# Optimization experiments

Measured on AMD Instinct MI355X. Metric: run time of the kernel, lower is better.

The kernel has to match this reference:

```python
import jax, jax.numpy as jnp
import numpy as np

NEG_SLOPE = 0.2
TAU_MRF = 1.0
N_NODES = 100000
PROJ_DIM = 128
GAT_DIM = 64
N_EDGES = 1000000


def setup_inputs() -> dict:
    key = jax.random.key(0)
    ks = jax.random.split(key, 8)
    z_beh = jax.random.normal(ks[0], (N_NODES, PROJ_DIM), dtype=jnp.float32)
    z_pref = jax.random.normal(ks[1], (N_NODES, PROJ_DIM), dtype=jnp.float32)
    edge_index = jax.random.randint(ks[2], (2, N_EDGES), 0, N_NODES, dtype=jnp.int64)
    # xavier_uniform for [GAT_DIM, PROJ_DIM] linear weights
    lim_w = float(np.sqrt(6.0 / (PROJ_DIM + GAT_DIM)))
    W_b = jax.random.uniform(ks[3], (GAT_DIM, PROJ_DIM), minval=-lim_w, maxval=lim_w, dtype=jnp.float32)
    W_p = jax.random.uniform(ks[4], (GAT_DIM, PROJ_DIM), minval=-lim_w, maxval=lim_w, dtype=jnp.float32)
    # xavier_uniform on view(1, 2D): fan_in=1? torch treats [1, 2D] -> fan_in=2D, fan_out=1
    lim_a = float(np.sqrt(6.0 / (1 + 2 * GAT_DIM)))
    a_b = jax.random.uniform(ks[5], (2 * GAT_DIM,), minval=-lim_a, maxval=lim_a, dtype=jnp.float32)
    a_p = jax.random.uniform(ks[6], (2 * GAT_DIM,), minval=-lim_a, maxval=lim_a, dtype=jnp.float32)
    gamma_b = jnp.zeros((), dtype=jnp.float32)
    gamma_p = jnp.zeros((), dtype=jnp.float32)
    return {"z_beh": z_beh, "z_pref": z_pref, "W_b": W_b, "W_p": W_p,
            "a_b": a_b, "a_p": a_p, "gamma_b": gamma_b, "gamma_p": gamma_p,
            "edge_index_undirected": edge_index}


def _sym_score(h, a, src, dst, neg_slope):
    # e_ij = leaky_relu((cat[h_src, h_dst]) . a). Split a to avoid materializing
    # the [E, 2D] concat: dot each node once, then gather scalars per edge.
    D = h.shape[-1]
    si = h @ a[:D]   # [N] contribution of left slot
    sj = h @ a[D:]   # [N] contribution of right slot
    e_ij = jax.nn.leaky_relu(si[src] + sj[dst], negative_slope=neg_slope)
    e_ji = jax.nn.leaky_relu(si[dst] + sj[src], negative_slope=neg_slope)
    return 0.5 * (e_ij + e_ji)


def reference(z_beh, z_pref, W_b, W_p, a_b, a_p, gamma_b, gamma_p, edge_index_undirected):
    src = edge_index_undirected[0]
    dst = edge_index_undirected[1]
    h_b = z_beh @ W_b.T   # [N, D]
    h_p = z_pref @ W_p.T  # [N, D]
    s_b = _sym_score(h_b, a_b, src, dst, NEG_SLOPE)  # [E]
    s_p = _sym_score(h_p, a_p, src, dst, NEG_SLOPE)  # [E]
    w = jax.nn.softmax(jnp.stack([gamma_b, gamma_p]))
    s = w[0] * s_b + w[1] * s_p
    alpha_ij = jax.nn.sigmoid(s / TAU_MRF)
    return alpha_ij
```

## Files before the change

### kernel.cpp

```cpp
#include <hip/hip_runtime.h>
#include <hip/hip_bf16.h>

#define NEG_SLOPE 0.2f

typedef float f32x4 __attribute__((ext_vector_type(4)));

__device__ __forceinline__ unsigned f2bf(float f) {
    unsigned u = __float_as_uint(f);
    return (u + 0x7FFFu + ((u >> 16) & 1u)) >> 16;
}
__device__ __forceinline__ float bf2f(unsigned h) {
    return __uint_as_float(h << 16);
}

__device__ __forceinline__ float fold_reduce(float sib, float sjb,
                                             float sip, float sjp,
                                             bool hiB, bool hiJ) {
    float g1 = hiB ? sib : sip;
    float r1 = __shfl_xor(g1, 16);
    float acc_i = (hiB ? sip : sib) + r1;
    float g2 = hiB ? sjb : sjp;
    float r2 = __shfl_xor(g2, 16);
    float acc_j = (hiB ? sjp : sjb) + r2;
    float g3 = hiJ ? acc_i : acc_j;
    float r3 = __shfl_xor(g3, 8);
    float acc = (hiJ ? acc_j : acc_i) + r3;
    acc += __shfl_xor(acc, 4);
    acc += __shfl_xor(acc, 2);
    acc += __shfl_xor(acc, 1);
    return acc;
}

__device__ __forceinline__ float dot4(const f32x4 z, const f32x4 v) {
    return z.x * v.x + z.y * v.y + z.z * v.z + z.w * v.w;
}

__device__ __forceinline__ void pack_store(float acc, int c, bool valid,
                                           uint2* __restrict__ tab8, int node) {
    const float a1 = __shfl_down(acc, 8);
    const float a2 = __shfl_down(acc, 16);
    const float a3 = __shfl_down(acc, 24);
    if (c == 0 && valid) {
        uint2 p;
        p.x = f2bf(acc) | (f2bf(a1) << 16);
        p.y = f2bf(a2) | (f2bf(a3) << 16);
        tab8[node] = p;
    }
}

__global__ void __launch_bounds__(1024) fused_node_kernel(
        const float* __restrict__ W_b,
        const float* __restrict__ W_p,
        const float* __restrict__ a_b,
        const float* __restrict__ a_p,
        const f32x4* __restrict__ zb4,
        const f32x4* __restrict__ zp4,
        uint2*       __restrict__ tab8,
        int n_nodes) {
    __shared__ float vsh[4][128];
    __shared__ float psh[1024];

    const int tid = threadIdx.x;
    {
        const int q   = tid >> 9;
        const int r   = tid & 511;
        const int vec = r >> 7;
        const int p   = r & 127;
        const float* W = (vec >= 2) ? W_p : W_b;
        const float* a = ((vec >= 2) ? a_p : a_b) + (vec & 1) * 64 + 32 * q;
        const float* Wc = W + (32 * q) * 128 + p;
        float acc = 0.f;
        #pragma unroll
        for (int k = 0; k < 32; ++k)
            acc += Wc[k * 128] * a[k];
        psh[tid] = acc;
    }
    __syncthreads();
    if (tid < 512)
        vsh[tid >> 7][tid & 127] = psh[tid] + psh[512 + tid];
    __syncthreads();

    const int lane = tid & 63;
    const int h    = lane >> 5;
    const int c    = lane & 31;
    const int wave   = (blockIdx.x * blockDim.x + tid) >> 6;
    const int nwaves = (gridDim.x * blockDim.x) >> 6;
    const int npairs = (n_nodes + 1) >> 1;

    const f32x4 v1b = *reinterpret_cast<const f32x4*>(&vsh[0][4 * c]);
    const f32x4 v2b = *reinterpret_cast<const f32x4*>(&vsh[1][4 * c]);
    const f32x4 v1p = *reinterpret_cast<const f32x4*>(&vsh[2][4 * c]);
    const f32x4 v2p = *reinterpret_cast<const f32x4*>(&vsh[3][4 * c]);

    const bool hiB = (c & 16) != 0;
    const bool hiJ = (c & 8)  != 0;

    for (int pr = wave; pr < npairs; pr += 2 * nwaves) {
        const int pr2 = pr + nwaves;
        int node1 = 2 * pr + h;
        const bool valid1 = node1 < n_nodes;
        if (!valid1) node1 = n_nodes - 1;
        const f32x4 zb1 = zb4[node1 * 32 + c];
        const f32x4 zp1 = zp4[node1 * 32 + c];
        int node2 = 2 * pr2 + h;
        const bool run2 = pr2 < npairs;
        bool valid2 = run2 && (node2 < n_nodes);
        if (!valid2) node2 = n_nodes - 1;
        const f32x4 zb2 = zb4[node2 * 32 + c];
        const f32x4 zp2 = zp4[node2 * 32 + c];

        float acc1 = fold_reduce(dot4(zb1, v1b), dot4(zb1, v2b),
                                 dot4(zp1, v1p), dot4(zp1, v2p), hiB, hiJ);
        pack_store(acc1, c, valid1, tab8, node1);

        float acc2 = fold_reduce(dot4(zb2, v1b), dot4(zb2, v2b),
                                 dot4(zp2, v1p), dot4(zp2, v2p), hiB, hiJ);
        pack_store(acc2, c, valid2, tab8, node2);
    }
}

__device__ __forceinline__ float lrelu(float x) {
    return x >= 0.f ? x : NEG_SLOPE * x;
}

__device__ __forceinline__ float edge_score8(const uint2 ts, const uint2 td,
                                             float w0, float w1) {
    const float s_ib = bf2f(ts.x & 0xFFFFu), s_jb = bf2f(ts.x >> 16);
    const float s_ip = bf2f(ts.y & 0xFFFFu), s_jp = bf2f(ts.y >> 16);
    const float d_ib = bf2f(td.x & 0xFFFFu), d_jb = bf2f(td.x >> 16);
    const float d_ip = bf2f(td.y & 0xFFFFu), d_jp = bf2f(td.y >> 16);
    const float sb = 0.5f * (lrelu(s_ib + d_jb) + lrelu(d_ib + s_jb));
    const float sp = 0.5f * (lrelu(s_ip + d_jp) + lrelu(d_ip + s_jp));
    const float sc = w0 * sb + w1 * sp;
    return 1.f / (1.f + __expf(-sc));
}

__global__ void __launch_bounds__(256) edge_scores_kernel(
        const int*   __restrict__ src,
        const int*   __restrict__ dst,
        const uint2* __restrict__ tab8,
        const float* __restrict__ gamma_b,
        const float* __restrict__ gamma_p,
        float*       __restrict__ out,
        int n_edges) {
    const float gb = *gamma_b;
    const float gp = *gamma_p;
    const float w0 = 1.f / (1.f + __expf(gp - gb));
    const float w1 = 1.f - w0;

    const int n_half = n_edges >> 1;
    const int stride = gridDim.x * blockDim.x;
    const int gid    = blockIdx.x * blockDim.x + threadIdx.x;

    const int2* src2 = (const int2*)src;
    const int2* dst2 = (const int2*)dst;
    float2*     out2 = (float2*)out;

    for (int i = gid; i < n_half; i += stride) {
        const int2 s = src2[i];
        const int2 d = dst2[i];
        const uint2 ts0 = tab8[s.x];
        const uint2 td0 = tab8[d.x];
        const uint2 ts1 = tab8[s.y];
        const uint2 td1 = tab8[d.y];
        float2 r;
        r.x = edge_score8(ts0, td0, w0, w1);
        r.y = edge_score8(ts1, td1, w0, w1);
        out2[i] = r;
    }
    const int tail_base = n_half << 1;
    for (int e = tail_base + gid; e < n_edges; e += stride) {
        out[e] = edge_score8(tab8[src[e]], tab8[dst[e]], w0, w1);
    }
}

extern "C" void kernel_launch(void* const* d_in, const int* in_sizes, int n_in,
                              void* d_out, int out_size, void* d_ws, size_t ws_size,
                              hipStream_t stream) {
    const float* z_beh  = (const float*)d_in[0];
    const float* z_pref = (const float*)d_in[1];
    const float* W_b    = (const float*)d_in[2];
    const float* W_p    = (const float*)d_in[3];
    const float* a_b    = (const float*)d_in[4];
    const float* a_p    = (const float*)d_in[5];
    const float* g_b    = (const float*)d_in[6];
    const float* g_p    = (const float*)d_in[7];
    const int*   ei     = (const int*)d_in[8];

    const int n_nodes = in_sizes[0] / 128;
    const int n_edges = in_sizes[8] / 2;

    uint2* tab8 = (uint2*)d_ws;

    fused_node_kernel<<<512, 1024, 0, stream>>>(
        W_b, W_p, a_b, a_p,
        (const f32x4*)z_beh, (const f32x4*)z_pref, tab8, n_nodes);

    const int n_half = n_edges >> 1;
    int eblocks = (n_half + 255) / 256;
    if (eblocks > 4096) eblocks = 4096;
    if (eblocks < 1) eblocks = 1;
    edge_scores_kernel<<<eblocks, 256, 0, stream>>>(
        ei, ei + n_edges, tab8, g_b, g_p, (float*)d_out, n_edges);
}
```

Before: 36.42 us.

## Split v precompute into separate kernel and unroll node loads four-deep

Moves the W·a folding out of the node kernel into a tiny single-block kernel that writes v to workspace. Every node block previously recomputed v and synchronised before streaming z, and the change removes that redundant work. The node kernel now uses 256-thread blocks with 2048 blocks and issues four pairs of row loads before computing, which raises memory-level parallelism. The cost is an extra kernel launch that the node kernel must wait on, plus global reads of v instead of shared memory.

```diff
diff --git a/kernel.cpp b/kernel.cpp
--- a/kernel.cpp
+++ b/kernel.cpp
@@ -11,6 +11,27 @@
 }
 __device__ __forceinline__ float bf2f(unsigned h) {
     return __uint_as_float(h << 16);
+}
+
+__global__ void compute_v_kernel(const float* __restrict__ W_b,
+                                 const float* __restrict__ W_p,
+                                 const float* __restrict__ a_b,
+                                 const float* __restrict__ a_p,
+                                 float* __restrict__ v) {
+    const int t  = threadIdx.x;
+    const int p  = t & 127;
+    const int ch = t >> 7;
+    const float* W = ch ? W_p : W_b;
+    const float* a = ch ? a_p : a_b;
+    float acc1 = 0.f, acc2 = 0.f;
+    #pragma unroll
+    for (int d = 0; d < 64; ++d) {
+        const float w = W[d * 128 + p];
+        acc1 += w * a[d];
+        acc2 += w * a[64 + d];
+    }
+    v[(2 * ch + 0) * 128 + p] = acc1;
+    v[(2 * ch + 1) * 128 + p] = acc2;
 }
 
 __device__ __forceinline__ float fold_reduce(float sib, float sjb,
@@ -48,38 +69,13 @@
     }
 }
 
-__global__ void __launch_bounds__(1024) fused_node_kernel(
-        const float* __restrict__ W_b,
-        const float* __restrict__ W_p,
-        const float* __restrict__ a_b,
-        const float* __restrict__ a_p,
+__global__ void __launch_bounds__(256, 8) node_scores_kernel(
         const f32x4* __restrict__ zb4,
         const f32x4* __restrict__ zp4,
+        const float* __restrict__ v,
         uint2*       __restrict__ tab8,
         int n_nodes) {
-    __shared__ float vsh[4][128];
-    __shared__ float psh[1024];
-
-    const int tid = threadIdx.x;
-    {
-        const int q   = tid >> 9;
-        const int r   = tid & 511;
-        const int vec = r >> 7;
-        const int p   = r & 127;
-        const float* W = (vec >= 2) ? W_p : W_b;
-        const float* a = ((vec >= 2) ? a_p : a_b) + (vec & 1) * 64 + 32 * q;
-        const float* Wc = W + (32 * q) * 128 + p;
-        float acc = 0.f;
-        #pragma unroll
-        for (int k = 0; k < 32; ++k)
-            acc += Wc[k * 128] * a[k];
-        psh[tid] = acc;
-    }
-    __syncthreads();
-    if (tid < 512)
-        vsh[tid >> 7][tid & 127] = psh[tid] + psh[512 + tid];
-    __syncthreads();
-
+    const int tid  = threadIdx.x;
     const int lane = tid & 63;
     const int h    = lane >> 5;
     const int c    = lane & 31;
@@ -87,35 +83,36 @@
     const int nwaves = (gridDim.x * blockDim.x) >> 6;
     const int npairs = (n_nodes + 1) >> 1;
 
-    const f32x4 v1b = *reinterpret_cast<const f32x4*>(&vsh[0][4 * c]);
-    const f32x4 v2b = *reinterpret_cast<const f32x4*>(&vsh[1][4 * c]);
-    const f32x4 v1p = *reinterpret_cast<const f32x4*>(&vsh[2][4 * c]);
-    const f32x4 v2p = *reinterpret_cast<const f32x4*>(&vsh[3][4 * c]);
+    const f32x4 v1b = *reinterpret_cast<const f32x4*>(v + 0 * 128 + 4 * c);
+    const f32x4 v2b = *reinterpret_cast<const f32x4*>(v + 1 * 128 + 4 * c);
+    const f32x4 v1p = *reinterpret_cast<const f32x4*>(v + 2 * 128 + 4 * c);
+    const f32x4 v2p = *reinterpret_cast<const f32x4*>(v + 3 * 128 + 4 * c);
 
     const bool hiB = (c & 16) != 0;
     const bool hiJ = (c & 8)  != 0;
 
-    for (int pr = wave; pr < npairs; pr += 2 * nwaves) {
-        const int pr2 = pr + nwaves;
-        int node1 = 2 * pr + h;
-        const bool valid1 = node1 < n_nodes;
-        if (!valid1) node1 = n_nodes - 1;
-        const f32x4 zb1 = zb4[node1 * 32 + c];
-        const f32x4 zp1 = zp4[node1 * 32 + c];
-        int node2 = 2 * pr2 + h;
-        const bool run2 = pr2 < npairs;
-        bool valid2 = run2 && (node2 < n_nodes);
-        if (!valid2) node2 = n_nodes - 1;
-        const f32x4 zb2 = zb4[node2 * 32 + c];
-        const f32x4 zp2 = zp4[node2 * 32 + c];
-
-        float acc1 = fold_reduce(dot4(zb1, v1b), dot4(zb1, v2b),
-                                 dot4(zp1, v1p), dot4(zp1, v2p), hiB, hiJ);
-        pack_store(acc1, c, valid1, tab8, node1);
-
-        float acc2 = fold_reduce(dot4(zb2, v1b), dot4(zb2, v2b),
-                                 dot4(zp2, v1p), dot4(zp2, v2p), hiB, hiJ);
-        pack_store(acc2, c, valid2, tab8, node2);
+    for (int pr0 = wave; pr0 < npairs; pr0 += 4 * nwaves) {
+        f32x4 zb[4], zp[4];
+        #pragma unroll
+        for (int j = 0; j < 4; ++j) {
+            const int pr = pr0 + j * nwaves;
+            if (pr < npairs) {
+                const size_t base = (size_t)(2 * pr + h) * 32 + c;
+                zb[j] = zb4[base];
+                zp[j] = zp4[base];
+            }
+        }
+        #pragma unroll
+        for (int j = 0; j < 4; ++j) {
+            const int pr = pr0 + j * nwaves;
+            if (pr < npairs) {
+                const int node = 2 * pr + h;
+                const float acc = fold_reduce(
+                    dot4(zb[j], v1b), dot4(zb[j], v2b),
+                    dot4(zp[j], v1p), dot4(zp[j], v2p), hiB, hiJ);
+                pack_store(acc, c, node < n_nodes, tab8, node);
+            }
+        }
     }
 }
 
@@ -190,11 +187,13 @@
     const int n_nodes = in_sizes[0] / 128;
     const int n_edges = in_sizes[8] / 2;
 
-    uint2* tab8 = (uint2*)d_ws;
-
-    fused_node_kernel<<<512, 1024, 0, stream>>>(
-        W_b, W_p, a_b, a_p,
-        (const f32x4*)z_beh, (const f32x4*)z_pref, tab8, n_nodes);
+    float* v    = (float*)d_ws;
+    uint2* tab8 = (uint2*)((char*)d_ws + 2048);
+
+    compute_v_kernel<<<1, 256, 0, stream>>>(W_b, W_p, a_b, a_p, v);
+
+    node_scores_kernel<<<2048, 256, 0, stream>>>(
+        (const f32x4*)z_beh, (const f32x4*)z_pref, v, tab8, n_nodes);
 
     const int n_half = n_edges >> 1;
     int eblocks = (n_half + 255) / 256;
```

New measurement: 41.41 us. 13.7% more time.
